# Kernel tuning notes

Measured on AMD Instinct MI355X. Metric: run time of the kernel, lower is better.

Reference implementation:

```python
import jax, jax.numpy as jnp
import numpy as np

C, H1, H2, K, HOUT = 128, 4, 5, 3, 4  # h_dim, gat1 heads, gat2 heads, BAN k, BAN h_out
BN_EPS = 1e-5


def _gat(x, W, a_src, a_dst, bias, src, dst, mask, N):
    # PyG-style GATConv: x:[N,Fin], W:[Fin,H*C], a_*:[H,C], mask:[E] (1=valid edge)
    H, Ch = a_src.shape
    xh = (x @ W).reshape(N, H, Ch)
    es = jnp.einsum('nhc,hc->nh', xh, a_src)
    ed = jnp.einsum('nhc,hc->nh', xh, a_dst)
    e = jax.nn.leaky_relu(es[src] + ed[dst], 0.2)                      # [E,H]
    e = jnp.where(mask[:, None] > 0, e, -1e9)
    m = jax.ops.segment_max(e, dst, num_segments=N)                    # [N,H]
    p = jnp.exp(e - m[dst]) * mask[:, None]
    s = jax.ops.segment_sum(p, dst, num_segments=N)
    alpha = p / s[dst]                                                 # segment softmax over incoming edges
    out = jax.ops.segment_sum(xh[src] * alpha[:, :, None], dst, num_segments=N)
    return out.reshape(N, H * Ch) + bias


def _forward(cell_features, Wd, bd, W1, a1s, a1d, b1, Wl1, bl1, W2, a2s, a2d, b2, Wl2, bl2,
             Wfc, bfc, Whg, bhg, Wc, bc, Wv, bv, Wq, bq, h_mat, h_bias, bn_gamma, bn_beta,
             triplets, edge_index):
    N = triplets.shape[0]
    src0, dst0 = edge_index[0], edge_index[1]
    # clean_edge_index drops self loops; GATConv (PyG default) re-adds exactly one per node
    idx = jnp.arange(N, dtype=src0.dtype)
    src = jnp.concatenate([src0, idx])
    dst = jnp.concatenate([dst0, idx])
    mask = jnp.concatenate([(src0 != dst0).astype(jnp.float32), jnp.ones((N,), jnp.float32)])
    x = triplets[:, :4].astype(jnp.float32) @ Wd + bd                  # drug_linear
    h1 = jax.nn.elu(_gat(x, W1, a1s, a1d, b1, src, dst, mask, N)) @ Wl1 + bl1
    h2 = jax.nn.elu(_gat(h1, W2, a2s, a2d, b2, src, dst, mask, N)) @ Wl2 + bl2
    h = jnp.mean(h1 + h2, axis=0)                                      # [C] graph readout
    hg = jax.nn.relu(h @ Wfc + bfc) @ Whg + bhg                        # [C]
    c = jax.nn.relu(cell_features @ Wc + bc)                           # [B,C]
    B = c.shape[0]
    v = jnp.broadcast_to(hg, (B, C))
    # BANLayer (DrugBAN) with singleton v/q sequence length
    v_ = jax.nn.relu(v @ Wv + bv)                                      # [B,C*K]
    q_ = jax.nn.relu(c @ Wq + bq)
    att = jnp.einsum('hk,bk,bk->bh', h_mat, v_, q_) + h_bias           # [B,HOUT]
    fused = att.sum(axis=1, keepdims=True) * (v_ * q_)                 # sum over heads of bilinear pooling
    logits = fused.reshape(B, C, K).sum(axis=-1)                       # AvgPool1d(k)*k == group sum
    mu = logits.mean(axis=0)
    var = logits.var(axis=0)                                           # biased var, as torch BN
    return (logits - mu) / jnp.sqrt(var + BN_EPS) * bn_gamma + bn_beta


def setup_inputs():
    key = jax.random.key(0)
    ks = iter(jax.random.split(key, 40))
    N, E, B, CF = 20000, 500000, 256, 954
    def w(shape, fan):
        return jax.random.normal(next(ks), shape, jnp.float32) / np.sqrt(fan)
    return dict(
        cell_features=jax.random.normal(next(ks), (B, CF), jnp.float32),
        Wd=w((4, C), 4), bd=jnp.zeros((C,), jnp.float32),
        W1=w((C, H1 * C), C), a1s=w((H1, C), C), a1d=w((H1, C), C), b1=jnp.zeros((H1 * C,), jnp.float32),
        Wl1=w((H1 * C, C), H1 * C), bl1=jnp.zeros((C,), jnp.float32),
        W2=w((C, H2 * C), C), a2s=w((H2, C), C), a2d=w((H2, C), C), b2=jnp.zeros((H2 * C,), jnp.float32),
        Wl2=w((H2 * C, C), H2 * C), bl2=jnp.zeros((C,), jnp.float32),
        Wfc=w((C, 2 * C), C), bfc=jnp.zeros((2 * C,), jnp.float32),
        Whg=w((2 * C, C), 2 * C), bhg=jnp.zeros((C,), jnp.float32),
        Wc=w((CF, C), CF), bc=jnp.zeros((C,), jnp.float32),
        Wv=w((C, C * K), C), bv=jnp.zeros((C * K,), jnp.float32),
        Wq=w((C, C * K), C), bq=jnp.zeros((C * K,), jnp.float32),
        h_mat=w((HOUT, C * K), C * K), h_bias=jnp.zeros((HOUT,), jnp.float32),
        bn_gamma=jnp.ones((C,), jnp.float32), bn_beta=jnp.zeros((C,), jnp.float32),
        triplets=jax.random.randint(next(ks), (N, 4), 0, 10, dtype=jnp.int32),
        edge_index=jax.random.randint(next(ks), (2, E), 0, N, dtype=jnp.int32),
    )


def reference(cell_features, Wd, bd, W1, a1s, a1d, b1, Wl1, bl1, W2, a2s, a2d, b2, Wl2, bl2,
              Wfc, bfc, Whg, bhg, Wc, bc, Wv, bv, Wq, bq, h_mat, h_bias, bn_gamma, bn_beta,
              triplets, edge_index):
    return _forward(cell_features, Wd, bd, W1, a1s, a1d, b1, Wl1, bl1, W2, a2s, a2d, b2, Wl2, bl2,
                    Wfc, bfc, Whg, bhg, Wc, bc, Wv, bv, Wq, bq, h_mat, h_bias, bn_gamma, bn_beta,
                    triplets, edge_index)
```

## Files before the change

kernel.cpp:

```cpp
#include <hip/hip_runtime.h>
#include <hip/hip_bf16.h>
#include <math.h>

#define CDIV(a,b) (((a)+(b)-1)/(b))

typedef __attribute__((ext_vector_type(8))) short short8v;
typedef __attribute__((ext_vector_type(4))) float f32x4;

__device__ inline float bf2lo(unsigned u) { return __uint_as_float(u << 16); }
__device__ inline float bf2hi(unsigned u) { return __uint_as_float(u & 0xffff0000u); }
__device__ inline float leaky(float v) { return v > 0.f ? v : 0.2f * v; }

__global__ void k_prep(const float* __restrict__ W1, __hip_bfloat16* __restrict__ W1t,
                       const float* __restrict__ Wl1, __hip_bfloat16* __restrict__ Wl1t,
                       const float* __restrict__ W2, __hip_bfloat16* __restrict__ W2t,
                       const float* __restrict__ Wl2, __hip_bfloat16* __restrict__ Wl2t,
                       const float* __restrict__ Wc, float* __restrict__ Wct,
                       const float* __restrict__ Wq, float* __restrict__ Wqt,
                       float* __restrict__ colsum, int* __restrict__ degz, int N) {
  int i = blockIdx.x * 256 + threadIdx.x;
  const int n1 = 128 * 512, n2 = 512 * 128, n3 = 128 * 640, n4 = 640 * 128;
  const int n5 = 954 * 128, n6 = 128 * 384;
  if (i < n1) { int m = i / 128, k = i % 128; W1t[i] = __float2bfloat16(W1[(size_t)k * 512 + m]); return; }
  i -= n1;
  if (i < n2) { int m = i / 512, k = i % 512; Wl1t[i] = __float2bfloat16(Wl1[(size_t)k * 128 + m]); return; }
  i -= n2;
  if (i < n3) { int m = i / 128, k = i % 128; W2t[i] = __float2bfloat16(W2[(size_t)k * 640 + m]); return; }
  i -= n3;
  if (i < n4) { int m = i / 640, k = i % 640; Wl2t[i] = __float2bfloat16(Wl2[(size_t)k * 128 + m]); return; }
  i -= n4;
  if (i < n5) { int m = i / 954, k = i % 954; Wct[i] = Wc[(size_t)k * 128 + m]; return; }
  i -= n5;
  if (i < n6) { int m = i / 128, k = i % 128; Wqt[i] = Wq[(size_t)k * 384 + m]; return; }
  i -= n6;
  if (i < 128) { colsum[i] = 0.f; return; }
  i -= 128;
  if (i < 2 * N) { degz[i] = 0; return; }
}

__global__ void k_degdrug(const int* __restrict__ src0, const int* __restrict__ dst0,
                          int* __restrict__ deg, int E,
                          const int* __restrict__ trip, const float* __restrict__ Wd,
                          const float* __restrict__ bd, __hip_bfloat16* __restrict__ x,
                          int N) {
  int i = blockIdx.x * 256 + threadIdx.x;
  if (i < E) {
    int s = src0[i], d = dst0[i];
    if (s != d) atomicAdd(&deg[d], 1);
    return;
  }
  i -= E;
  if (i >= N * 128) return;
  int n = i >> 7, c = i & 127;
  const int* t = trip + n * 4;
  float acc = bd[c];
  acc += (float)t[0] * Wd[c] + (float)t[1] * Wd[128 + c] +
         (float)t[2] * Wd[256 + c] + (float)t[3] * Wd[384 + c];
  x[i] = __float2bfloat16(acc);
}

template <bool BIAS, bool COLSUM>
__global__ void k_gemm_mfma(const __hip_bfloat16* __restrict__ A,
                            const __hip_bfloat16* __restrict__ Bt,
                            const float* __restrict__ bias,
                            __hip_bfloat16* __restrict__ Cb,
                            float* __restrict__ colsum,
                            int Nr, int K, int M) {
  __shared__ short As[64 * 40];
  __shared__ short Bs[64 * 40];
  int tid = threadIdx.x;
  int lane = tid & 63, wid = tid >> 6;
  int wr = wid >> 1, wc = wid & 1;
  int lrow = lane & 15;
  int row0 = blockIdx.y * 64, col0 = blockIdx.x * 64;

  int arow = tid >> 2, akc = tid & 3;
  int grow = row0 + arow; if (grow >= Nr) grow = Nr - 1;
  const __hip_bfloat16* agp = A + (size_t)grow * K + akc * 8;
  const __hip_bfloat16* bgp = Bt + (size_t)(col0 + arow) * K + akc * 8;
  short* asp = &As[arow * 40 + akc * 8];
  short* bsp = &Bs[arow * 40 + akc * 8];

  f32x4 acc00 = {0.f,0.f,0.f,0.f}, acc01 = acc00, acc10 = acc00, acc11 = acc00;

  int lkc = lane >> 4;
  const short* a0p = &As[(wr * 32 + lrow) * 40 + lkc * 8];
  const short* a1p = &As[(wr * 32 + 16 + lrow) * 40 + lkc * 8];
  const short* b0p = &Bs[(wc * 32 + lrow) * 40 + lkc * 8];
  const short* b1p = &Bs[(wc * 32 + 16 + lrow) * 40 + lkc * 8];

  for (int k0 = 0; k0 < K; k0 += 32) {
    short8v av = *(const short8v*)(agp + k0);
    short8v bv = *(const short8v*)(bgp + k0);
    __syncthreads();
    *(short8v*)asp = av;
    *(short8v*)bsp = bv;
    __syncthreads();
    short8v a0 = *(const short8v*)a0p;
    short8v a1 = *(const short8v*)a1p;
    short8v b0 = *(const short8v*)b0p;
    short8v b1 = *(const short8v*)b1p;
    acc00 = __builtin_amdgcn_mfma_f32_16x16x32_bf16(a0, b0, acc00, 0, 0, 0);
    acc01 = __builtin_amdgcn_mfma_f32_16x16x32_bf16(a0, b1, acc01, 0, 0, 0);
    acc10 = __builtin_amdgcn_mfma_f32_16x16x32_bf16(a1, b0, acc10, 0, 0, 0);
    acc11 = __builtin_amdgcn_mfma_f32_16x16x32_bf16(a1, b1, acc11, 0, 0, 0);
  }

  int rbase = row0 + wr * 32 + (lane >> 4) * 4;
  int cbase = col0 + wc * 32 + lrow;
  float part0 = 0.f, part1 = 0.f;
#pragma unroll
  for (int m = 0; m < 2; ++m) {
#pragma unroll
    for (int n = 0; n < 2; ++n) {
      f32x4 acc = m == 0 ? (n == 0 ? acc00 : acc01) : (n == 0 ? acc10 : acc11);
      int col = cbase + n * 16;
      int plane = col >> 7, ch = col & 127;
      float bv = BIAS ? bias[col] : 0.f;
      __hip_bfloat16* cp = Cb + (size_t)plane * Nr * 128 + ch;
#pragma unroll
      for (int r = 0; r < 4; ++r) {
        int grow2 = rbase + m * 16 + r;
        if (grow2 >= Nr) continue;
        float v = acc[r] + bv;
        cp[(size_t)grow2 * 128] = __float2bfloat16(v);
        if (COLSUM) { if (n == 0) part0 += v; else part1 += v; }
      }
    }
  }
  if (COLSUM) {
    part0 += __shfl_xor(part0, 16); part0 += __shfl_xor(part0, 32);
    part1 += __shfl_xor(part1, 16); part1 += __shfl_xor(part1, 32);
    if (lane < 16) {
      atomicAdd(&colsum[cbase], part0);
      atomicAdd(&colsum[cbase + 16], part1);
    }
  }
}

__global__ void k_dotmm(const float* __restrict__ A, const float* __restrict__ Bt,
                        const float* __restrict__ bias, float* __restrict__ C,
                        int Nr, int K, int M) {
  int wid = (blockIdx.x * blockDim.x + threadIdx.x) >> 6;
  int lane = threadIdx.x & 63;
  if (wid >= Nr * M) return;
  int b = wid / M, m = wid % M;
  const float* ar = A + (size_t)b * K;
  const float* br = Bt + (size_t)m * K;
  float acc = 0.f;
  for (int k = lane * 2; k + 1 < K; k += 128) {
    float2 av = *(const float2*)(ar + k);
    float2 bv = *(const float2*)(br + k);
    acc += av.x * bv.x + av.y * bv.y;
  }
#pragma unroll
  for (int off = 32; off; off >>= 1) acc += __shfl_xor(acc, off);
  if (lane == 0) C[wid] = fmaxf(acc + bias[m], 0.f);
}

__global__ void k_coef(const __hip_bfloat16* __restrict__ xh, const float* __restrict__ as_,
                       const float* __restrict__ ad_, float* __restrict__ es,
                       float* __restrict__ ed, int N) {
  int h = blockIdx.y;
  int n = blockIdx.x * 4 + (threadIdx.x >> 6);
  int lane = threadIdx.x & 63;
  if (n >= N) return;
  const __hip_bfloat162* xp = (const __hip_bfloat162*)xh + ((size_t)h * N + n) * 64;
  __hip_bfloat162 xv = xp[lane];
  float x0 = __bfloat162float(xv.x), x1 = __bfloat162float(xv.y);
  float2 a = ((const float2*)(as_ + h * 128))[lane];
  float2 d = ((const float2*)(ad_ + h * 128))[lane];
  float e1 = x0 * a.x + x1 * a.y;
  float e2 = x0 * d.x + x1 * d.y;
#pragma unroll
  for (int off = 32; off; off >>= 1) {
    e1 += __shfl_xor(e1, off);
    e2 += __shfl_xor(e2, off);
  }
  if (lane == 0) { es[(size_t)h * N + n] = e1; ed[(size_t)h * N + n] = e2; }
}

__global__ void k_scan(const int* __restrict__ deg, int* __restrict__ rowptr, int N) {
  __shared__ int part[1024];
  int t = threadIdx.x;
  int chunk = (N + 1023) >> 10;
  int b0 = t * chunk, b1 = min(N, b0 + chunk);
  int s = 0;
  for (int i = b0; i < b1; i++) s += deg[i];
  part[t] = s;
  __syncthreads();
  for (int off = 1; off < 1024; off <<= 1) {
    int v = (t >= off) ? part[t - off] : 0;
    __syncthreads();
    part[t] += v;
    __syncthreads();
  }
  int run = (t == 0) ? 0 : part[t - 1];
  for (int i = b0; i < b1; i++) { rowptr[i] = run; run += deg[i]; }
  if (b1 == N) rowptr[N] = run;
}

__global__ void k_fill_adj(const int* __restrict__ src0, const int* __restrict__ dst0,
                           const int* __restrict__ rowptr, int* __restrict__ cursor,
                           int* __restrict__ adj, int E) {
  int e = blockIdx.x * 256 + threadIdx.x;
  if (e >= E) return;
  int s = src0[e], d = dst0[e];
  if (s != d) {
    int pos = rowptr[d] + atomicAdd(&cursor[d], 1);
    adj[pos] = s;
  }
}

__device__ __forceinline__ void acc8p(const char* xbase, int loff, unsigned pk, int j,
                                      float& a0, float& a1) {
  unsigned k0 = __builtin_amdgcn_readlane(pk, j);
  unsigned k1 = __builtin_amdgcn_readlane(pk, j + 1);
  unsigned k2 = __builtin_amdgcn_readlane(pk, j + 2);
  unsigned k3 = __builtin_amdgcn_readlane(pk, j + 3);
  unsigned k4 = __builtin_amdgcn_readlane(pk, j + 4);
  unsigned k5 = __builtin_amdgcn_readlane(pk, j + 5);
  unsigned k6 = __builtin_amdgcn_readlane(pk, j + 6);
  unsigned k7 = __builtin_amdgcn_readlane(pk, j + 7);
  unsigned u0 = *(const unsigned*)(xbase + (size_t)(k0 & 0x7FFFu) * 256 + loff);
  unsigned u1 = *(const unsigned*)(xbase + (size_t)(k1 & 0x7FFFu) * 256 + loff);
  unsigned u2 = *(const unsigned*)(xbase + (size_t)(k2 & 0x7FFFu) * 256 + loff);
  unsigned u3 = *(const unsigned*)(xbase + (size_t)(k3 & 0x7FFFu) * 256 + loff);
  unsigned u4 = *(const unsigned*)(xbase + (size_t)(k4 & 0x7FFFu) * 256 + loff);
  unsigned u5 = *(const unsigned*)(xbase + (size_t)(k5 & 0x7FFFu) * 256 + loff);
  unsigned u6 = *(const unsigned*)(xbase + (size_t)(k6 & 0x7FFFu) * 256 + loff);
  unsigned u7 = *(const unsigned*)(xbase + (size_t)(k7 & 0x7FFFu) * 256 + loff);
  float p0 = __uint_as_float(k0 & 0xFFFF0000u);
  float p1 = __uint_as_float(k1 & 0xFFFF0000u);
  float p2 = __uint_as_float(k2 & 0xFFFF0000u);
  float p3 = __uint_as_float(k3 & 0xFFFF0000u);
  float p4 = __uint_as_float(k4 & 0xFFFF0000u);
  float p5 = __uint_as_float(k5 & 0xFFFF0000u);
  float p6 = __uint_as_float(k6 & 0xFFFF0000u);
  float p7 = __uint_as_float(k7 & 0xFFFF0000u);
  a0 += p0 * bf2lo(u0); a1 += p0 * bf2hi(u0);
  a0 += p1 * bf2lo(u1); a1 += p1 * bf2hi(u1);
  a0 += p2 * bf2lo(u2); a1 += p2 * bf2hi(u2);
  a0 += p3 * bf2lo(u3); a1 += p3 * bf2hi(u3);
  a0 += p4 * bf2lo(u4); a1 += p4 * bf2hi(u4);
  a0 += p5 * bf2lo(u5); a1 += p5 * bf2hi(u5);
  a0 += p6 * bf2lo(u6); a1 += p6 * bf2hi(u6);
  a0 += p7 * bf2lo(u7); a1 += p7 * bf2hi(u7);
}

__global__ void k_gat_gather(const int* __restrict__ rowptr, const int* __restrict__ adj,
                             const float* __restrict__ es, const float* __restrict__ ed,
                             const __hip_bfloat16* __restrict__ xh,
                             const float* __restrict__ bias,
                             __hip_bfloat16* __restrict__ gout, int N, int H) {
  int nb = gridDim.x, bx = blockIdx.x;
  int sb = ((nb & 7) == 0) ? ((bx & 7) * (nb >> 3) + (bx >> 3)) : bx;
  int h = blockIdx.y;
  int n = sb * 4 + (threadIdx.x >> 6);
  int lane = threadIdx.x & 63;
  if (n >= N) return;
  int base = rowptr[n];
  int deg = rowptr[n + 1] - base;
  const float* esh = es + (size_t)h * N;
  float edn = ed[(size_t)h * N + n];
  float vself = leaky(esh[n] + edn);
  const char* xbase = (const char*)xh + (size_t)h * N * 256;
  int loff = lane * 4;

  float a0 = 0.f, a1 = 0.f;
  float psum = 0.f, pself, m;

  if (deg <= 64) {
    int s = 0; float v = -3e38f;
    if (lane < deg) { s = adj[base + lane]; v = leaky(esh[s] + edn); }
    m = fmaxf(vself, v);
#pragma unroll
    for (int off = 32; off; off >>= 1) m = fmaxf(m, __shfl_xor(m, off));
    float p = (lane < deg) ? __expf(v - m) : 0.f;
    pself = __expf(vself - m);
    psum = p;
    unsigned pk = (__float_as_uint(p) & 0xFFFF0000u) | (unsigned)s;
    for (int j = 0; j < deg; j += 8) acc8p(xbase, loff, pk, j, a0, a1);
  } else {
    m = vself;
    for (int i = lane; i < deg; i += 64) {
      int s = adj[base + i];
      m = fmaxf(m, leaky(esh[s] + edn));
    }
#pragma unroll
    for (int off = 32; off; off >>= 1) m = fmaxf(m, __shfl_xor(m, off));
    pself = __expf(vself - m);
    for (int c = 0; c < deg; c += 64) {
      int i = c + lane;
      int s = 0; float p = 0.f;
      if (i < deg) {
        s = adj[base + i];
        p = __expf(leaky(esh[s] + edn) - m);
        psum += p;
      }
      unsigned pk = (__float_as_uint(p) & 0xFFFF0000u) | (unsigned)s;
      int cnt = min(64, deg - c);
      for (int j = 0; j < cnt; j += 8) acc8p(xbase, loff, pk, j, a0, a1);
    }
  }

  {
    unsigned u = *(const unsigned*)(xbase + (size_t)n * 256 + loff);
    a0 += pself * bf2lo(u);
    a1 += pself * bf2hi(u);
  }
#pragma unroll
  for (int off = 32; off; off >>= 1) psum += __shfl_xor(psum, off);
  psum += pself;
  float inv = 1.f / psum;
  float2 bv = ((const float2*)(bias + h * 128))[lane];
  float o0 = a0 * inv + bv.x;
  float o1 = a1 * inv + bv.y;
  o0 = o0 > 0.f ? o0 : __expf(o0) - 1.f;
  o1 = o1 > 0.f ? o1 : __expf(o1) - 1.f;
  __hip_bfloat162 r;
  r.x = __float2bfloat16(o0);
  r.y = __float2bfloat16(o1);
  ((__hip_bfloat162*)(gout + (size_t)n * (H * 128) + h * 128))[lane] = r;
}

__global__ void k_head(const float* __restrict__ colsum, const float* __restrict__ Wfc,
                       const float* __restrict__ bfc, const float* __restrict__ Whg,
                       const float* __restrict__ bhg, const float* __restrict__ Wv,
                       const float* __restrict__ bv, float* __restrict__ vvec, float invN) {
  __shared__ float h[128], t1[256], hg[128];
  int t = threadIdx.x;
  if (t < 128) h[t] = colsum[t] * invN;
  __syncthreads();
  float acc = bfc[t];
  for (int k = 0; k < 128; k++) acc += h[k] * Wfc[k * 256 + t];
  t1[t] = fmaxf(acc, 0.f);
  __syncthreads();
  if (t < 128) {
    float a2 = bhg[t];
    for (int k = 0; k < 256; k++) a2 += t1[k] * Whg[k * 128 + t];
    hg[t] = a2;
  }
  __syncthreads();
  for (int j = t; j < 384; j += 256) {
    float a3 = bv[j];
    for (int k = 0; k < 128; k++) a3 += hg[k] * Wv[k * 384 + j];
    vvec[j] = fmaxf(a3, 0.f);
  }
}

__global__ void k_fused(const float* __restrict__ vvec, const float* __restrict__ q,
                        const float* __restrict__ hmat, const float* __restrict__ hbias,
                        float* __restrict__ logits) {
  int b = blockIdx.x, c = threadIdx.x;
  __shared__ float red[128];
  float t[3];
  float part = 0.f;
#pragma unroll
  for (int j = 0; j < 3; j++) {
    int k = c * 3 + j;
    float hs = hmat[k] + hmat[384 + k] + hmat[768 + k] + hmat[1152 + k];
    t[j] = vvec[k] * q[(size_t)b * 384 + k];
    part += hs * t[j];
  }
  red[c] = part;
  __syncthreads();
  for (int s = 64; s > 0; s >>= 1) {
    if (c < s) red[c] += red[c + s];
    __syncthreads();
  }
  float attsum = red[0] + (hbias[0] + hbias[1] + hbias[2] + hbias[3]);
  logits[(size_t)b * 128 + c] = attsum * (t[0] + t[1] + t[2]);
}

__global__ void k_bn(const float* __restrict__ logits, const float* __restrict__ gamma,
                     const float* __restrict__ beta, float* __restrict__ out, int B) {
  int c = blockIdx.x, b = threadIdx.x;
  __shared__ float s1[256], s2[256];
  float v = logits[(size_t)b * 128 + c];
  s1[b] = v; s2[b] = v * v;
  __syncthreads();
  for (int s = B / 2; s > 0; s >>= 1) {
    if (b < s) { s1[b] += s1[b + s]; s2[b] += s2[b + s]; }
    __syncthreads();
  }
  float mu = s1[0] / B;
  float var = s2[0] / B - mu * mu;
  out[(size_t)b * 128 + c] = (v - mu) * rsqrtf(var + 1e-5f) * gamma[c] + beta[c];
}

extern "C" void kernel_launch(void* const* d_in, const int* in_sizes, int n_in,
                              void* d_out, int out_size, void* d_ws, size_t ws_size,
                              hipStream_t stream) {
  const float* cell = (const float*)d_in[0];
  const float* Wd   = (const float*)d_in[1];
  const float* bd   = (const float*)d_in[2];
  const float* W1   = (const float*)d_in[3];
  const float* a1s  = (const float*)d_in[4];
  const float* a1d  = (const float*)d_in[5];
  const float* b1   = (const float*)d_in[6];
  const float* Wl1  = (const float*)d_in[7];
  const float* bl1  = (const float*)d_in[8];
  const float* W2   = (const float*)d_in[9];
  const float* a2s  = (const float*)d_in[10];
  const float* a2d  = (const float*)d_in[11];
  const float* b2   = (const float*)d_in[12];
  const float* Wl2  = (const float*)d_in[13];
  const float* bl2  = (const float*)d_in[14];
  const float* Wfc  = (const float*)d_in[15];
  const float* bfc  = (const float*)d_in[16];
  const float* Whg  = (const float*)d_in[17];
  const float* bhg  = (const float*)d_in[18];
  const float* Wc   = (const float*)d_in[19];
  const float* bc   = (const float*)d_in[20];
  const float* Wv   = (const float*)d_in[21];
  const float* bv   = (const float*)d_in[22];
  const float* Wq   = (const float*)d_in[23];
  const float* bq   = (const float*)d_in[24];
  const float* hmat = (const float*)d_in[25];
  const float* hbias= (const float*)d_in[26];
  const float* gamma= (const float*)d_in[27];
  const float* beta = (const float*)d_in[28];
  const int* trip   = (const int*)d_in[29];
  const int* eidx   = (const int*)d_in[30];

  const int N = in_sizes[29] / 4;
  const int E = in_sizes[30] / 2;
  const int B = in_sizes[0] / 954;
  float* out = (float*)d_out;

  __hip_bfloat16* xb    = (__hip_bfloat16*)d_ws;
  __hip_bfloat16* xhb   = xb + (size_t)N * 128;
  __hip_bfloat16* goutb = xhb + (size_t)N * 640;
  __hip_bfloat16* h1b   = goutb + (size_t)N * 640;
  __hip_bfloat16* h2b   = h1b + (size_t)N * 128;
  __hip_bfloat16* W1t   = h2b + (size_t)N * 128;
  __hip_bfloat16* Wl1t  = W1t + 512 * 128;
  __hip_bfloat16* W2t   = Wl1t + 128 * 512;
  __hip_bfloat16* Wl2t  = W2t + 640 * 128;
  float* es     = (float*)(Wl2t + 128 * 640);
  float* ed     = es + (size_t)N * 5;
  float* colsum = ed + (size_t)N * 5;
  float* cbuf   = colsum + 128;
  float* qbuf   = cbuf + (size_t)B * 128;
  float* vvec   = qbuf + (size_t)B * 384;
  float* logits = vvec + 384;
  float* Wct    = logits + (size_t)B * 128;
  float* Wqt    = Wct + 128 * 954;
  int* rowptr   = (int*)(Wqt + 384 * 128);
  int* degb     = rowptr + (N + 1);
  int* cursor   = degb + N;
  int* adj      = cursor + N;

  const int* src0 = eidx;
  const int* dst0 = eidx + E;

  {
    int tot = 128*512 + 512*128 + 128*640 + 640*128 + 954*128 + 128*384 + 128 + 2 * N;
    k_prep<<<CDIV(tot, 256), 256, 0, stream>>>(W1, W1t, Wl1, Wl1t, W2, W2t, Wl2, Wl2t,
                                               Wc, Wct, Wq, Wqt, colsum, degb, N);
  }

  k_degdrug<<<CDIV(E + N * 128, 256), 256, 0, stream>>>(src0, dst0, degb, E,
                                                        trip, Wd, bd, xb, N);
  k_scan<<<1, 1024, 0, stream>>>(degb, rowptr, N);
  k_fill_adj<<<CDIV(E, 256), 256, 0, stream>>>(src0, dst0, rowptr, cursor, adj, E);

  {
    dim3 g(512 / 64, CDIV(N, 64));
    k_gemm_mfma<false, false><<<g, 256, 0, stream>>>(xb, W1t, nullptr, xhb, nullptr, N, 128, 512);
  }
  {
    dim3 g(CDIV(N, 4), 4);
    k_coef<<<g, 256, 0, stream>>>(xhb, a1s, a1d, es, ed, N);
    k_gat_gather<<<g, 256, 0, stream>>>(rowptr, adj, es, ed, xhb, b1, goutb, N, 4);
  }
  {
    dim3 g(128 / 64, CDIV(N, 64));
    k_gemm_mfma<true, true><<<g, 256, 0, stream>>>(goutb, Wl1t, bl1, h1b, colsum, N, 512, 128);
  }

  {
    dim3 g(640 / 64, CDIV(N, 64));
    k_gemm_mfma<false, false><<<g, 256, 0, stream>>>(h1b, W2t, nullptr, xhb, nullptr, N, 128, 640);
  }
  {
    dim3 g(CDIV(N, 4), 5);
    k_coef<<<g, 256, 0, stream>>>(xhb, a2s, a2d, es, ed, N);
    k_gat_gather<<<g, 256, 0, stream>>>(rowptr, adj, es, ed, xhb, b2, goutb, N, 5);
  }
  {
    dim3 g(128 / 64, CDIV(N, 64));
    k_gemm_mfma<true, true><<<g, 256, 0, stream>>>(goutb, Wl2t, bl2, h2b, colsum, N, 640, 128);
  }

  k_head<<<1, 256, 0, stream>>>(colsum, Wfc, bfc, Whg, bhg, Wv, bv, vvec, 1.0f / N);
  k_dotmm<<<CDIV(B * 128, 4), 256, 0, stream>>>(cell, Wct, bc, cbuf, B, 954, 128);
  k_dotmm<<<CDIV(B * 384, 4), 256, 0, stream>>>(cbuf, Wqt, bq, qbuf, B, 128, 384);
  k_fused<<<B, 128, 0, stream>>>(vvec, qbuf, hmat, hbias, logits);
  k_bn<<<128, B, 0, stream>>>(logits, gamma, beta, out, B);
}
```

Baseline: 483.6 us.

## Fuse GAT attention coefficient computation into GEMM epilogue and prefetch next K tile

Removes the separate k_coef kernels by computing per-node, per-head source and destination attention dot products inside the feature GEMM epilogue, reducing partial sums with shuffles and atomics into es/ed buffers. The prep kernel now zeroes these buffers, and each layer gets separate buffers. The GEMM main loop also loads the next K tile into registers before the MFMAs to overlap global loads with compute. Costs are extra float atomics per row, non-deterministic summation order, and higher register pressure in the epilogue.

```diff
diff --git a/kernel.cpp b/kernel.cpp
--- a/kernel.cpp
+++ b/kernel.cpp
@@ -17,7 +17,8 @@
                        const float* __restrict__ Wl2, __hip_bfloat16* __restrict__ Wl2t,
                        const float* __restrict__ Wc, float* __restrict__ Wct,
                        const float* __restrict__ Wq, float* __restrict__ Wqt,
-                       float* __restrict__ colsum, int* __restrict__ degz, int N) {
+                       float* __restrict__ colsum, int* __restrict__ degz,
+                       float* __restrict__ esz, int N) {
   int i = blockIdx.x * 256 + threadIdx.x;
   const int n1 = 128 * 512, n2 = 512 * 128, n3 = 128 * 640, n4 = 640 * 128;
   const int n5 = 954 * 128, n6 = 128 * 384;
@@ -36,6 +37,8 @@
   if (i < 128) { colsum[i] = 0.f; return; }
   i -= 128;
   if (i < 2 * N) { degz[i] = 0; return; }
+  i -= 2 * N;
+  if (i < 18 * N) { esz[i] = 0.f; return; }
 }
 
 __global__ void k_degdrug(const int* __restrict__ src0, const int* __restrict__ dst0,
@@ -59,12 +62,14 @@
   x[i] = __float2bfloat16(acc);
 }
 
-template <bool BIAS, bool COLSUM>
+template <bool BIAS, bool COLSUM, bool COEF>
 __global__ void k_gemm_mfma(const __hip_bfloat16* __restrict__ A,
                             const __hip_bfloat16* __restrict__ Bt,
                             const float* __restrict__ bias,
                             __hip_bfloat16* __restrict__ Cb,
                             float* __restrict__ colsum,
+                            const float* __restrict__ as_, const float* __restrict__ ad_,
+                            float* __restrict__ es, float* __restrict__ ed,
                             int Nr, int K, int M) {
   __shared__ short As[64 * 40];
   __shared__ short Bs[64 * 40];
@@ -89,13 +94,17 @@
   const short* b0p = &Bs[(wc * 32 + lrow) * 40 + lkc * 8];
   const short* b1p = &Bs[(wc * 32 + 16 + lrow) * 40 + lkc * 8];
 
+  short8v av = *(const short8v*)agp;
+  short8v bv = *(const short8v*)bgp;
   for (int k0 = 0; k0 < K; k0 += 32) {
-    short8v av = *(const short8v*)(agp + k0);
-    short8v bv = *(const short8v*)(bgp + k0);
     __syncthreads();
     *(short8v*)asp = av;
     *(short8v*)bsp = bv;
     __syncthreads();
+    if (k0 + 32 < K) {
+      av = *(const short8v*)(agp + k0 + 32);
+      bv = *(const short8v*)(bgp + k0 + 32);
+    }
     short8v a0 = *(const short8v*)a0p;
     short8v a1 = *(const short8v*)a1p;
     short8v b0 = *(const short8v*)b0p;
@@ -108,7 +117,21 @@
 
   int rbase = row0 + wr * 32 + (lane >> 4) * 4;
   int cbase = col0 + wc * 32 + lrow;
+  int hplane = col0 >> 7;
   float part0 = 0.f, part1 = 0.f;
+  float esp[2][4], edp[2][4];
+  float as0, as1, ad0, ad1;
+  if (COEF) {
+#pragma unroll
+    for (int m = 0; m < 2; ++m)
+#pragma unroll
+      for (int r = 0; r < 4; ++r) { esp[m][r] = 0.f; edp[m][r] = 0.f; }
+    int ch0 = (cbase & 127);
+    as0 = as_[hplane * 128 + ch0];
+    as1 = as_[hplane * 128 + ch0 + 16];
+    ad0 = ad_[hplane * 128 + ch0];
+    ad1 = ad_[hplane * 128 + ch0 + 16];
+  }
 #pragma unroll
   for (int m = 0; m < 2; ++m) {
 #pragma unroll
@@ -116,15 +139,19 @@
       f32x4 acc = m == 0 ? (n == 0 ? acc00 : acc01) : (n == 0 ? acc10 : acc11);
       int col = cbase + n * 16;
       int plane = col >> 7, ch = col & 127;
-      float bv = BIAS ? bias[col] : 0.f;
+      float bv2 = BIAS ? bias[col] : 0.f;
       __hip_bfloat16* cp = Cb + (size_t)plane * Nr * 128 + ch;
 #pragma unroll
       for (int r = 0; r < 4; ++r) {
         int grow2 = rbase + m * 16 + r;
         if (grow2 >= Nr) continue;
-        float v = acc[r] + bv;
+        float v = acc[r] + bv2;
         cp[(size_t)grow2 * 128] = __float2bfloat16(v);
         if (COLSUM) { if (n == 0) part0 += v; else part1 += v; }
+        if (COEF) {
+          esp[m][r] += v * (n == 0 ? as0 : as1);
+          edp[m][r] += v * (n == 0 ? ad0 : ad1);
+        }
       }
     }
   }
@@ -134,6 +161,26 @@
     if (lane < 16) {
       atomicAdd(&colsum[cbase], part0);
       atomicAdd(&colsum[cbase + 16], part1);
+    }
+  }
+  if (COEF) {
+#pragma unroll
+    for (int m = 0; m < 2; ++m) {
+#pragma unroll
+      for (int r = 0; r < 4; ++r) {
+        float e = esp[m][r], d = edp[m][r];
+        e += __shfl_xor(e, 1); e += __shfl_xor(e, 2);
+        e += __shfl_xor(e, 4); e += __shfl_xor(e, 8);
+        d += __shfl_xor(d, 1); d += __shfl_xor(d, 2);
+        d += __shfl_xor(d, 4); d += __shfl_xor(d, 8);
+        if ((lane & 15) == 0) {
+          int grow2 = rbase + m * 16 + r;
+          if (grow2 < Nr) {
+            atomicAdd(&es[(size_t)hplane * Nr + grow2], e);
+            atomicAdd(&ed[(size_t)hplane * Nr + grow2], d);
+          }
+        }
+      }
     }
   }
 }
@@ -156,28 +203,6 @@
 #pragma unroll
   for (int off = 32; off; off >>= 1) acc += __shfl_xor(acc, off);
   if (lane == 0) C[wid] = fmaxf(acc + bias[m], 0.f);
-}
-
-__global__ void k_coef(const __hip_bfloat16* __restrict__ xh, const float* __restrict__ as_,
-                       const float* __restrict__ ad_, float* __restrict__ es,
-                       float* __restrict__ ed, int N) {
-  int h = blockIdx.y;
-  int n = blockIdx.x * 4 + (threadIdx.x >> 6);
-  int lane = threadIdx.x & 63;
-  if (n >= N) return;
-  const __hip_bfloat162* xp = (const __hip_bfloat162*)xh + ((size_t)h * N + n) * 64;
-  __hip_bfloat162 xv = xp[lane];
-  float x0 = __bfloat162float(xv.x), x1 = __bfloat162float(xv.y);
-  float2 a = ((const float2*)(as_ + h * 128))[lane];
-  float2 d = ((const float2*)(ad_ + h * 128))[lane];
-  float e1 = x0 * a.x + x1 * a.y;
-  float e2 = x0 * d.x + x1 * d.y;
-#pragma unroll
-  for (int off = 32; off; off >>= 1) {
-    e1 += __shfl_xor(e1, off);
-    e2 += __shfl_xor(e2, off);
-  }
-  if (lane == 0) { es[(size_t)h * N + n] = e1; ed[(size_t)h * N + n] = e2; }
 }
 
 __global__ void k_scan(const int* __restrict__ deg, int* __restrict__ rowptr, int N) {
@@ -438,9 +463,11 @@
   __hip_bfloat16* Wl1t  = W1t + 512 * 128;
   __hip_bfloat16* W2t   = Wl1t + 128 * 512;
   __hip_bfloat16* Wl2t  = W2t + 640 * 128;
-  float* es     = (float*)(Wl2t + 128 * 640);
-  float* ed     = es + (size_t)N * 5;
-  float* colsum = ed + (size_t)N * 5;
+  float* es1    = (float*)(Wl2t + 128 * 640);
+  float* ed1    = es1 + (size_t)4 * N;
+  float* es2    = ed1 + (size_t)4 * N;
+  float* ed2    = es2 + (size_t)5 * N;
+  float* colsum = ed2 + (size_t)5 * N;
   float* cbuf   = colsum + 128;
   float* qbuf   = cbuf + (size_t)B * 128;
   float* vvec   = qbuf + (size_t)B * 384;
@@ -456,9 +483,10 @@
   const int* dst0 = eidx + E;
 
   {
-    int tot = 128*512 + 512*128 + 128*640 + 640*128 + 954*128 + 128*384 + 128 + 2 * N;
+    int tot = 128*512 + 512*128 + 128*640 + 640*128 + 954*128 + 128*384
+              + 128 + 2 * N + 18 * N;
     k_prep<<<CDIV(tot, 256), 256, 0, stream>>>(W1, W1t, Wl1, Wl1t, W2, W2t, Wl2, Wl2t,
-                                               Wc, Wct, Wq, Wqt, colsum, degb, N);
+                                               Wc, Wct, Wq, Wqt, colsum, degb, es1, N);
   }
 
   k_degdrug<<<CDIV(E + N * 128, 256), 256, 0, stream>>>(src0, dst0, degb, E,
@@ -468,30 +496,32 @@
 
   {
     dim3 g(512 / 64, CDIV(N, 64));
-    k_gemm_mfma<false, false><<<g, 256, 0, stream>>>(xb, W1t, nullptr, xhb, nullptr, N, 128, 512);
+    k_gemm_mfma<false, false, true><<<g, 256, 0, stream>>>(
+        xb, W1t, nullptr, xhb, nullptr, a1s, a1d, es1, ed1, N, 128, 512);
   }
   {
     dim3 g(CDIV(N, 4), 4);
-    k_coef<<<g, 256, 0, stream>>>(xhb, a1s, a1d, es, ed, N);
-    k_gat_gather<<<g, 256, 0, stream>>>(rowptr, adj, es, ed, xhb, b1, goutb, N, 4);
+    k_gat_gather<<<g, 256, 0, stream>>>(rowptr, adj, es1, ed1, xhb, b1, goutb, N, 4);
   }
   {
     dim3 g(128 / 64, CDIV(N, 64));
-    k_gemm_mfma<true, true><<<g, 256, 0, stream>>>(goutb, Wl1t, bl1, h1b, colsum, N, 512, 128);
+    k_gemm_mfma<true, true, false><<<g, 256, 0, stream>>>(
+        goutb, Wl1t, bl1, h1b, colsum, nullptr, nullptr, nullptr, nullptr, N, 512, 128);
   }
 
   {
     dim3 g(640 / 64, CDIV(N, 64));
-    k_gemm_mfma<false, false><<<g, 256, 0, stream>>>(h1b, W2t, nullptr, xhb, nullptr, N, 128, 640);
+    k_gemm_mfma<false, false, true><<<g, 256, 0, stream>>>(
+        h1b, W2t, nullptr, xhb, nullptr, a2s, a2d, es2, ed2, N, 128, 640);
   }
   {
     dim3 g(CDIV(N, 4), 5);
-    k_coef<<<g, 256, 0, stream>>>(xhb, a2s, a2d, es, ed, N);
-    k_gat_gather<<<g, 256, 0, stream>>>(rowptr, adj, es, ed, xhb, b2, goutb, N, 5);
+    k_gat_gather<<<g, 256, 0, stream>>>(rowptr, adj, es2, ed2, xhb, b2, goutb, N, 5);
   }
   {
     dim3 g(128 / 64, CDIV(N, 64));
-    k_gemm_mfma<true, true><<<g, 256, 0, stream>>>(goutb, Wl2t, bl2, h2b, colsum, N, 640, 128);
+    k_gemm_mfma<true, true, false><<<g, 256, 0, stream>>>(
+        goutb, Wl2t, bl2, h2b, colsum, nullptr, nullptr, nullptr, nullptr, N, 640, 128);
   }
 
   k_head<<<1, 256, 0, stream>>>(colsum, Wfc, bfc, Whg, bhg, Wv, bv, vvec, 1.0f / N);
```

Result: no change. 475.6 us (-1.7%).
